# Kernel tuning notes

Measured on AMD Instinct MI355X. Metric: run time of the kernel, lower is better.

## Reference

```python
import jax, jax.numpy as jnp
import numpy as np

EMBEDS = 195  # C, also used in the (unusual) 1/sqrt(C) scale


def setup_inputs() -> dict:
    key = jax.random.key(0)
    k1, k2, k3, k4 = jax.random.split(key, 4)
    B, T, C, H = 1024, 256, EMBEDS, 8
    x = jax.random.normal(k1, (B, T, C), dtype=jnp.float32)
    Wq = jax.random.normal(k2, (C, H), dtype=jnp.float32) * 0.05
    Wk = jax.random.normal(k3, (C, H), dtype=jnp.float32) * 0.05
    Wv = jax.random.normal(k4, (C, H), dtype=jnp.float32) * 0.05
    return {"x": x, "Wq": Wq, "Wk": Wk, "Wv": Wv}


def reference(x, Wq, Wk, Wv):
    B, T, C = x.shape
    q = jnp.einsum('btc,ch->bth', x, Wq)  # [B,T,H]
    k = jnp.einsum('btc,ch->bth', x, Wk)
    v = jnp.einsum('btc,ch->bth', x, Wv)
    # scores scaled by 1/sqrt(C) (embedding dim), faithful to source
    scores = jnp.einsum('bqh,bkh->bqk', q, k) * (1.0 / jnp.sqrt(jnp.float32(C)))
    causal = jnp.tril(jnp.ones((T, T), dtype=bool))  # [T,T]
    scores = jnp.where(causal, scores, -jnp.inf)
    attn = jax.nn.softmax(scores, axis=-1)
    # dropout treated as identity (eval mode) for deterministic reference
    out = jnp.einsum('bqk,bkh->bqh', attn, v)
    return out
```

## Files before the change

### kernel.cpp

```cpp
#include <hip/hip_runtime.h>
#include <hip/hip_bf16.h>
#include <stdint.h>

#define TT   256
#define CC   195
#define HH   8
#define QSTR 24
#define NKT  7

typedef __attribute__((ext_vector_type(8))) short short8;
typedef __attribute__((ext_vector_type(4))) float f32x4;

static __device__ __forceinline__ short f2bf(float v) {
    union { __hip_bfloat16 h; short s; } cv;
    cv.h = __float2bfloat16(v);
    return cv.s;
}

__global__ __launch_bounds__(256, 4)
void fused_head(const float* __restrict__ x,
                const float* __restrict__ Wq,
                const float* __restrict__ Wk,
                const float* __restrict__ Wv,
                float* __restrict__ out)
{
    __shared__ float qkv[TT * QSTR];

    const int tid  = threadIdx.x;
    const int lane = tid & 63;
    const int wv   = __builtin_amdgcn_readfirstlane(tid >> 6);
    const int b    = blockIdx.x;
    const int nn   = lane & 15;
    const int quad = lane >> 4;

    const float* __restrict__ xb = x + (size_t)b * (TT * CC);

    const float* Wsel0 = (nn < 8) ? (Wq + nn) : (Wk + nn - 8);
    const float* Wsel1 = (nn < 8) ? (Wv + nn) : nullptr;
    short8 Bf[NKT][2];
#pragma unroll
    for (int kt = 0; kt < NKT; ++kt) {
#pragma unroll
        for (int j = 0; j < 8; ++j) {
            const int k = kt * 32 + quad * 8 + j;
            float v0 = (k < CC) ? Wsel0[(size_t)k * HH] : 0.f;
            float v1 = (k < CC && Wsel1) ? Wsel1[(size_t)k * HH] : 0.f;
            Bf[kt][0][j] = f2bf(v0);
            Bf[kt][1][j] = f2bf(v1);
        }
    }

    for (int ch = 0; ch < 4; ++ch) {
        const int rbase = ch * 64 + wv * 16;
        const float* __restrict__ xrow = xb + (size_t)(rbase + nn) * CC;

        f32x4 acc0 = {0.f, 0.f, 0.f, 0.f};
        f32x4 acc1 = {0.f, 0.f, 0.f, 0.f};
#pragma unroll
        for (int kt = 0; kt < NKT; ++kt) {
            float f[8];
#pragma unroll
            for (int j = 0; j < 8; ++j) {
                const int k = kt * 32 + quad * 8 + j;
                f[j] = (k < CC) ? xrow[k] : 0.f;
            }
            short8 a;
#pragma unroll
            for (int j = 0; j < 8; ++j) a[j] = f2bf(f[j]);
            acc0 = __builtin_amdgcn_mfma_f32_16x16x32_bf16(a, Bf[kt][0], acc0, 0, 0, 0);
            acc1 = __builtin_amdgcn_mfma_f32_16x16x32_bf16(a, Bf[kt][1], acc1, 0, 0, 0);
        }
#pragma unroll
        for (int r = 0; r < 4; ++r) {
            const int trow = rbase + quad * 4 + r;
            qkv[trow * QSTR + nn] = acc0[r];
            if (nn < 8)
                qkv[trow * QSTR + 16 + nn] = acc1[r];
        }
    }
    __syncthreads();

    const int t = tid;
    const float4 q0 = *reinterpret_cast<const float4*>(qkv + t * QSTR);
    const float4 q1 = *reinterpret_cast<const float4*>(qkv + t * QSTR + 4);
    float o0 = 0.f, o1 = 0.f, o2 = 0.f, o3 = 0.f;
    float o4 = 0.f, o5 = 0.f, o6 = 0.f, o7 = 0.f;
    float denom = 0.f;
    const float SCALE = 0.07161149f;
    const int jmax = (wv + 1) * 64;
    for (int j = 0; j < jmax; j += 4) {
        const float* kv = qkv + j * QSTR;
        float s[4];
#pragma unroll
        for (int u = 0; u < 4; ++u) {
            const float4 k0 = *reinterpret_cast<const float4*>(kv + u * QSTR + 8);
            const float4 k1 = *reinterpret_cast<const float4*>(kv + u * QSTR + 12);
            s[u] = q0.x * k0.x + q0.y * k0.y + q0.z * k0.z + q0.w * k0.w
                 + q1.x * k1.x + q1.y * k1.y + q1.z * k1.z + q1.w * k1.w;
        }
        float e[4];
#pragma unroll
        for (int u = 0; u < 4; ++u) {
            e[u] = (j + u <= t) ? __expf(s[u] * SCALE) : 0.f;
            denom += e[u];
        }
#pragma unroll
        for (int u = 0; u < 4; ++u) {
            const float4 v0 = *reinterpret_cast<const float4*>(kv + u * QSTR + 16);
            const float4 v1 = *reinterpret_cast<const float4*>(kv + u * QSTR + 20);
            o0 = fmaf(e[u], v0.x, o0); o1 = fmaf(e[u], v0.y, o1);
            o2 = fmaf(e[u], v0.z, o2); o3 = fmaf(e[u], v0.w, o3);
            o4 = fmaf(e[u], v1.x, o4); o5 = fmaf(e[u], v1.y, o5);
            o6 = fmaf(e[u], v1.z, o6); o7 = fmaf(e[u], v1.w, o7);
        }
    }
    const float inv = 1.0f / denom;
    float* op = out + ((size_t)b * TT + t) * HH;
    *reinterpret_cast<float4*>(op)     = make_float4(o0 * inv, o1 * inv, o2 * inv, o3 * inv);
    *reinterpret_cast<float4*>(op + 4) = make_float4(o4 * inv, o5 * inv, o6 * inv, o7 * inv);
}

extern "C" void kernel_launch(void* const* d_in, const int* in_sizes, int n_in,
                              void* d_out, int out_size, void* d_ws, size_t ws_size,
                              hipStream_t stream)
{
    const float* x  = (const float*)d_in[0];
    const float* Wq = (const float*)d_in[1];
    const float* Wk = (const float*)d_in[2];
    const float* Wv = (const float*)d_in[3];
    float* out      = (float*)d_out;
    const int B = in_sizes[0] / (TT * CC);
    fused_head<<<dim3(B), dim3(256), 0, stream>>>(x, Wq, Wk, Wv, out);
}
```

Baseline: 315.0 us.

## Move attention scores and PV product onto bf16 MFMA with balanced query tiles

Replaces the per-thread scalar fp32 attention loop with MFMA-based QK^T and P·V in bf16. Q, K and transposed V are stored in LDS as bf16, and probabilities are staged per wave in LDS. A row of ones appended to Vt makes the MFMA also produce the softmax denominator. Query tiles are assigned in a balanced pattern (wv, 7-wv, 8+wv, 15-wv) so causal work is even across waves. This cuts scalar FMA and exp work and LDS traffic, but adds bf16 rounding of the scores, probabilities and V, and wastes MFMA lanes because only a K dimension of 8 is used.

```diff
diff --git a/kernel.cpp b/kernel.cpp
--- a/kernel.cpp
+++ b/kernel.cpp
@@ -5,8 +5,9 @@
 #define TT   256
 #define CC   195
 #define HH   8
-#define QSTR 24
 #define NKT  7
+#define VSTR 260
+#define PSTR 40
 
 typedef __attribute__((ext_vector_type(8))) short short8;
 typedef __attribute__((ext_vector_type(4))) float f32x4;
@@ -24,7 +25,10 @@
                 const float* __restrict__ Wv,
                 float* __restrict__ out)
 {
-    __shared__ float qkv[TT * QSTR];
+    __shared__ short Ql[TT * 8];
+    __shared__ short Kl[TT * 8];
+    __shared__ short Vt[16 * VSTR];
+    __shared__ short Pch[4 * 16 * PSTR];
 
     const int tid  = threadIdx.x;
     const int lane = tid & 63;
@@ -32,6 +36,13 @@
     const int b    = blockIdx.x;
     const int nn   = lane & 15;
     const int quad = lane >> 4;
+
+    {
+        uint32_t* vtw = (uint32_t*)Vt;
+        const int base = (8 * VSTR) / 2;
+        for (int i = tid; i < (8 * VSTR) / 2; i += 256)
+            vtw[base + i] = (i < VSTR / 2) ? 0x3F803F80u : 0u;
+    }
 
     const float* __restrict__ xb = x + (size_t)b * (TT * CC);
 
@@ -73,51 +84,64 @@
 #pragma unroll
         for (int r = 0; r < 4; ++r) {
             const int trow = rbase + quad * 4 + r;
-            qkv[trow * QSTR + nn] = acc0[r];
-            if (nn < 8)
-                qkv[trow * QSTR + 16 + nn] = acc1[r];
+            const short qs = f2bf(acc0[r]);
+            if (nn < 8) {
+                Ql[trow * 8 + nn] = qs;
+                Vt[nn * VSTR + trow] = f2bf(acc1[r]);
+            } else {
+                Kl[trow * 8 + (nn - 8)] = qs;
+            }
         }
     }
     __syncthreads();
 
-    const int t = tid;
-    const float4 q0 = *reinterpret_cast<const float4*>(qkv + t * QSTR);
-    const float4 q1 = *reinterpret_cast<const float4*>(qkv + t * QSTR + 4);
-    float o0 = 0.f, o1 = 0.f, o2 = 0.f, o3 = 0.f;
-    float o4 = 0.f, o5 = 0.f, o6 = 0.f, o7 = 0.f;
-    float denom = 0.f;
-    const float SCALE = 0.07161149f;
-    const int jmax = (wv + 1) * 64;
-    for (int j = 0; j < jmax; j += 4) {
-        const float* kv = qkv + j * QSTR;
-        float s[4];
+    const float SC2 = 0.07161149f * 1.44269504f;
+    const int qt4[4] = { wv, 7 - wv, 8 + wv, 15 - wv };
+    short* Pw = Pch + wv * (16 * PSTR);
+
+    for (int qi = 0; qi < 4; ++qi) {
+        const int qt = qt4[qi];
+        const int qb = qt * 16;
+
+        short8 aQ = (short8){0, 0, 0, 0, 0, 0, 0, 0};
+        if (quad == 0)
+            aQ = *reinterpret_cast<const short8*>(Ql + (qb + nn) * 8);
+
+        f32x4 accO = {0.f, 0.f, 0.f, 0.f};
+        const int nch = (qt >> 1) + 1;
+        for (int c = 0; c < nch; ++c) {
+            const int kb = c * 32;
+            asm volatile("" ::: "memory");
 #pragma unroll
-        for (int u = 0; u < 4; ++u) {
-            const float4 k0 = *reinterpret_cast<const float4*>(kv + u * QSTR + 8);
-            const float4 k1 = *reinterpret_cast<const float4*>(kv + u * QSTR + 12);
-            s[u] = q0.x * k0.x + q0.y * k0.y + q0.z * k0.z + q0.w * k0.w
-                 + q1.x * k1.x + q1.y * k1.y + q1.z * k1.z + q1.w * k1.w;
-        }
-        float e[4];
+            for (int half = 0; half < 2; ++half) {
+                const int kb16 = kb + half * 16;
+                short8 bK = (short8){0, 0, 0, 0, 0, 0, 0, 0};
+                if (quad == 0)
+                    bK = *reinterpret_cast<const short8*>(Kl + (kb16 + nn) * 8);
+                f32x4 s = __builtin_amdgcn_mfma_f32_16x16x32_bf16(
+                              aQ, bK, (f32x4){0.f, 0.f, 0.f, 0.f}, 0, 0, 0);
+                const int key = kb16 + nn;
 #pragma unroll
-        for (int u = 0; u < 4; ++u) {
-            e[u] = (j + u <= t) ? __expf(s[u] * SCALE) : 0.f;
-            denom += e[u];
+                for (int r = 0; r < 4; ++r) {
+                    const int qrow = qb + quad * 4 + r;
+                    const float e = (key <= qrow) ? exp2f(s[r] * SC2) : 0.f;
+                    Pw[(quad * 4 + r) * PSTR + half * 16 + nn] = f2bf(e);
+                }
+            }
+            asm volatile("s_waitcnt lgkmcnt(0)" ::: "memory");
+            const short8 aP = *reinterpret_cast<const short8*>(Pw + nn * PSTR + quad * 8);
+            const short8 bV = *reinterpret_cast<const short8*>(Vt + nn * VSTR + kb + quad * 8);
+            accO = __builtin_amdgcn_mfma_f32_16x16x32_bf16(aP, bV, accO, 0, 0, 0);
         }
 #pragma unroll
-        for (int u = 0; u < 4; ++u) {
-            const float4 v0 = *reinterpret_cast<const float4*>(kv + u * QSTR + 16);
-            const float4 v1 = *reinterpret_cast<const float4*>(kv + u * QSTR + 20);
-            o0 = fmaf(e[u], v0.x, o0); o1 = fmaf(e[u], v0.y, o1);
-            o2 = fmaf(e[u], v0.z, o2); o3 = fmaf(e[u], v0.w, o3);
-            o4 = fmaf(e[u], v1.x, o4); o5 = fmaf(e[u], v1.y, o5);
-            o6 = fmaf(e[u], v1.z, o6); o7 = fmaf(e[u], v1.w, o7);
+        for (int r = 0; r < 4; ++r) {
+            const float dn = __shfl(accO[r], (lane & 48) | 8);
+            if (nn < 8) {
+                const int qrow = qb + quad * 4 + r;
+                out[((size_t)b * TT + qrow) * HH + nn] = accO[r] / dn;
+            }
         }
     }
-    const float inv = 1.0f / denom;
-    float* op = out + ((size_t)b * TT + t) * HH;
-    *reinterpret_cast<float4*>(op)     = make_float4(o0 * inv, o1 * inv, o2 * inv, o3 * inv);
-    *reinterpret_cast<float4*>(op + 4) = make_float4(o4 * inv, o5 * inv, o6 * inv, o7 * inv);
 }
 
 extern "C" void kernel_launch(void* const* d_in, const int* in_sizes, int n_in,
```

New measurement: 306.2 us. 2.8% less time.
